# Performance work log

Hardware: AMD Instinct MI355X
Metric: run time of the kernel (lower is better)

Reference implementation:

```python
import jax, jax.numpy as jnp
import numpy as np

N_NODES = 50000
N_EDGES = 800000
DIM = 128


def setup_inputs() -> dict:
    key = jax.random.key(0)
    k_x, k_e, k_w1, k_w2 = jax.random.split(key, 4)
    x = jax.random.normal(k_x, (N_NODES, DIM), dtype=jnp.float32)
    edge_index = jax.random.randint(k_e, (2, N_EDGES), 0, N_NODES, dtype=jnp.int64)
    scale = 1.0 / np.sqrt(DIM)
    W1 = jax.random.normal(k_w1, (DIM, DIM), dtype=jnp.float32) * scale
    b1 = jnp.zeros((DIM,), dtype=jnp.float32)
    W2 = jax.random.normal(k_w2, (DIM, DIM), dtype=jnp.float32) * scale
    b2 = jnp.zeros((DIM,), dtype=jnp.float32)
    return {"x": x, "edge_index": edge_index, "W1": W1, "b1": b1, "W2": W2, "b2": b2}


def _gcn_conv(x, W, b, src, dst, n_nodes):
    """PyG GCNConv: D^{-1/2}(A+I)D^{-1/2} (x @ W) + b, self-loops added."""
    h = x @ W  # [N, D]
    ones = jnp.ones(src.shape[0], dtype=h.dtype)
    # degree of A+I, counting incoming edges at target nodes plus self-loop
    deg = jax.ops.segment_sum(ones, dst, num_segments=n_nodes) + 1.0
    dinv = jax.lax.rsqrt(deg)  # [N]
    norm = dinv[src] * dinv[dst]  # [E]
    msgs = h[src] * norm[:, None]  # [E, D] gather (memory-bound)
    agg = jax.ops.segment_sum(msgs, dst, num_segments=n_nodes)  # scatter-add
    agg = agg + h * (dinv * dinv)[:, None]  # self-loop contribution
    return agg + b


def reference(x, edge_index, W1, b1, W2, b2):
    src, dst = edge_index[0], edge_index[1]
    n = x.shape[0]
    identity = x
    out = jax.nn.relu(_gcn_conv(x, W1, b1, src, dst, n))
    out = _gcn_conv(out, W2, b2, src, dst, n)
    return jax.nn.relu(out + identity)
```

## Files before the change

kernel.cpp:

```cpp
#include <hip/hip_runtime.h>

#define N_NODES 50000
#define N_EDGES 800000
#define DIM 128
#define NB 391
#define CAP 2560
#define NCH 7
#define BIN_CHUNK 4096
#define BIN_BLOCKS 196

typedef unsigned int uint;
typedef unsigned short ushort;
typedef __attribute__((ext_vector_type(8))) __bf16 bf16x8;
typedef __attribute__((ext_vector_type(4))) float f32x4;

__device__ __forceinline__ uint f2bf(float f) {
    uint u = __float_as_uint(f);
    return (u + 0x7FFFu + ((u >> 16) & 1u)) >> 16;
}
__device__ __forceinline__ float2 bf2f2(uint u) {
    return make_float2(__uint_as_float(u << 16), __uint_as_float(u & 0xFFFF0000u));
}


__global__ __launch_bounds__(256) void prep_kernel(const float* __restrict__ W1,
                                                   const float* __restrict__ W2,
                                                   uint* __restrict__ Wt1,
                                                   uint* __restrict__ Wt2,
                                                   int* __restrict__ bincursor) {
    int idx = blockIdx.x * 256 + threadIdx.x;
    if (idx < 16384) {
        const float* W = (idx < 8192) ? W1 : W2;
        uint* Wt = (idx < 8192) ? Wt1 : Wt2;
        int i = idx & 8191;
        int n = i >> 6, k2 = i & 63;
        uint lo = f2bf(W[(2 * k2) * DIM + n]);
        uint hi = f2bf(W[(2 * k2 + 1) * DIM + n]);
        Wt[i] = lo | (hi << 16);
    } else {
        int b = idx - 16384;
        if (b < NB) bincursor[b] = b * CAP;
    }
}


__global__ __launch_bounds__(256) void bin_kernel(const int* __restrict__ ei,
                                                  int* __restrict__ bincursor,
                                                  uint* __restrict__ pairs) {
    __shared__ int lh[NB];
    __shared__ int lbase[NB];
    int t = threadIdx.x;
    int eb = blockIdx.x * BIN_CHUNK;

    for (int b = t; b < NB; b += 256) lh[b] = 0;
    __syncthreads();

    int s_reg[16], d_reg[16];
#pragma unroll
    for (int i = 0; i < 16; ++i) {
        int e = eb + i * 256 + t;
        if (e < N_EDGES) {
            s_reg[i] = ei[e];
            d_reg[i] = ei[N_EDGES + e];
            atomicAdd(&lh[d_reg[i] >> 7], 1);
        } else {
            d_reg[i] = -1;
        }
    }
    __syncthreads();

    for (int b = t; b < NB; b += 256) {
        int c = lh[b];
        lbase[b] = c ? atomicAdd(&bincursor[b], c) : 0;
    }
    __syncthreads();
    for (int b = t; b < NB; b += 256) lh[b] = 0;
    __syncthreads();

#pragma unroll
    for (int i = 0; i < 16; ++i) {
        int d = d_reg[i];
        if (d >= 0) {
            int bin = d >> 7;
            int r = atomicAdd(&lh[bin], 1);
            pairs[lbase[bin] + r] = ((uint)s_reg[i] << 7) | (uint)(d & 127);
        }
    }
}


__global__ __launch_bounds__(256) void fill2_kernel(const uint* __restrict__ pairs,
                                                    const int* __restrict__ bincursor,
                                                    int* __restrict__ rowbeg,
                                                    int* __restrict__ rowend,
                                                    float* __restrict__ dinv,
                                                    int* __restrict__ csr_src) {
    __shared__ int cnt[128 * 8];
    __shared__ int nsum[128];
    __shared__ int nbase[128];
    int t = threadIdx.x;
    int blk = blockIdx.x;
    int bs = blk * CAP;
    int be = bincursor[blk];

    for (int i = t; i < 128 * 8; i += 256) cnt[i] = 0;
    __syncthreads();

    for (int p = bs + t; p < be; p += 256) {
        uint pr = pairs[p];
        atomicAdd(&cnt[(pr & 127u) * 8 + (pr >> 20)], 1);
    }
    __syncthreads();

    if (t < 128) {
        int s = 0;
#pragma unroll
        for (int c = 0; c < NCH; ++c) s += cnt[t * 8 + c];
        nsum[t] = s;
        nbase[t] = s;
    }
    __syncthreads();
#pragma unroll
    for (int off = 1; off < 128; off <<= 1) {
        int v = (t < 128 && t >= off) ? nbase[t - off] : 0;
        __syncthreads();
        if (t < 128) nbase[t] += v;
        __syncthreads();
    }

    if (t < 128) {
        int ex = nbase[t] - nsum[t];
        int node = blk * 128 + t;
        if (node < N_NODES) {
            rowbeg[node] = bs + ex;
            rowend[node] = bs + nbase[t];
            dinv[node] = rsqrtf((float)nsum[t] + 1.0f);
        }
        int run = ex;
#pragma unroll
        for (int c = 0; c < NCH; ++c) {
            int v = cnt[t * 8 + c];
            cnt[t * 8 + c] = run;
            run += v;
        }
    }
    __syncthreads();

    for (int p = bs + t; p < be; p += 256) {
        uint pr = pairs[p];
        int r = atomicAdd(&cnt[(pr & 127u) * 8 + (pr >> 20)], 1);
        csr_src[bs + r] = (int)(pr >> 7);
    }
}


template <bool ABF>
__global__ __launch_bounds__(256) void mgemm_kernel(const void* __restrict__ Xv,
                                                    const uint* __restrict__ Wt,
                                                    const float* __restrict__ dinv,
                                                    uint* __restrict__ Hs) {
    int t = threadIdx.x;
    int wv = t >> 6;
    int l = t & 63;
    int col = l & 15;
    int g = l >> 4;
    int r0 = blockIdx.x * 64 + wv * 16;

    int ar = r0 + col;
    if (ar > N_NODES - 1) ar = N_NODES - 1;

    bf16x8 a[4];
    if (ABF) {
        const uint4* Xr = (const uint4*)((const uint*)Xv + (size_t)ar * 64);
#pragma unroll
        for (int kk = 0; kk < 4; ++kk) a[kk] = __builtin_bit_cast(bf16x8, Xr[kk * 4 + g]);
    } else {
        const float4* Xr = (const float4*)((const float*)Xv + (size_t)ar * DIM);
#pragma unroll
        for (int kk = 0; kk < 4; ++kk) {
            float4 x0 = Xr[kk * 8 + g * 2];
            float4 x1 = Xr[kk * 8 + g * 2 + 1];
            uint4 p;
            p.x = f2bf(x0.x) | (f2bf(x0.y) << 16);
            p.y = f2bf(x0.z) | (f2bf(x0.w) << 16);
            p.z = f2bf(x1.x) | (f2bf(x1.y) << 16);
            p.w = f2bf(x1.z) | (f2bf(x1.w) << 16);
            a[kk] = __builtin_bit_cast(bf16x8, p);
        }
    }

    const uint4* Wr = (const uint4*)Wt;
    f32x4 acc[8];
#pragma unroll
    for (int n = 0; n < 8; ++n) acc[n] = (f32x4){0.f, 0.f, 0.f, 0.f};

#pragma unroll
    for (int n = 0; n < 8; ++n) {
        const uint4* wrow = Wr + (size_t)(n * 16 + col) * 16;
#pragma unroll
        for (int kk = 0; kk < 4; ++kk) {
            bf16x8 b = __builtin_bit_cast(bf16x8, wrow[kk * 4 + g]);
            acc[n] = __builtin_amdgcn_mfma_f32_16x16x32_bf16(a[kk], b, acc[n], 0, 0, 0);
        }
    }

#pragma unroll
    for (int j = 0; j < 4; ++j) {
        int row = r0 + g * 4 + j;
        if (row < N_NODES) {
            float di = dinv[row];
            ushort* hrow = (ushort*)(Hs + (size_t)row * 64);
#pragma unroll
            for (int n = 0; n < 8; ++n) {
                hrow[n * 16 + col] = (ushort)f2bf(acc[n][j] * di);
            }
        }
    }
}


template <bool RES, bool OBF>
__global__ __launch_bounds__(256) void agg_kernel(const int* __restrict__ rowbeg,
                                                  const int* __restrict__ rowend,
                                                  const int* __restrict__ csr_src,
                                                  const uint* __restrict__ Hs,
                                                  const float* __restrict__ dinv,
                                                  const float* __restrict__ b,
                                                  const float* __restrict__ resid,
                                                  void* __restrict__ outv) {
    int wave = (int)((blockIdx.x * (size_t)blockDim.x + threadIdx.x) >> 6);
    int lane = threadIdx.x & 63;
    int grp = lane >> 4;
    int li = lane & 15;
    int node = wave * 4 + grp;

    int beg = rowbeg[node];
    int end = rowend[node];

    const uint4* H4 = (const uint4*)Hs;
    float a0, a1, a2, a3, a4, a5, a6, a7;
    {
        uint4 su = H4[(size_t)node * 16 + li];
        float2 v0 = bf2f2(su.x), v1 = bf2f2(su.y), v2 = bf2f2(su.z), v3 = bf2f2(su.w);
        a0 = v0.x; a1 = v0.y; a2 = v1.x; a3 = v1.y;
        a4 = v2.x; a5 = v2.y; a6 = v3.x; a7 = v3.y;
    }

#define ADD8(u)                                                                   \
    {                                                                             \
        float2 v0 = bf2f2(u.x), v1 = bf2f2(u.y), v2 = bf2f2(u.z), v3 = bf2f2(u.w);\
        a0 += v0.x; a1 += v0.y; a2 += v1.x; a3 += v1.y;                           \
        a4 += v2.x; a5 += v2.y; a6 += v3.x; a7 += v3.y;                           \
    }

    int e = beg;
    for (; e + 3 < end; e += 4) {
        int s0 = csr_src[e], s1 = csr_src[e + 1], s2 = csr_src[e + 2], s3 = csr_src[e + 3];
        uint4 u0 = H4[(size_t)s0 * 16 + li];
        uint4 u1 = H4[(size_t)s1 * 16 + li];
        uint4 u2 = H4[(size_t)s2 * 16 + li];
        uint4 u3 = H4[(size_t)s3 * 16 + li];
        ADD8(u0);
        ADD8(u1);
        ADD8(u2);
        ADD8(u3);
    }
    for (; e < end; ++e) {
        int s = csr_src[e];
        uint4 u = H4[(size_t)s * 16 + li];
        ADD8(u);
    }
#undef ADD8

    float di = dinv[node];
    const float4* B4 = (const float4*)b;
    float4 bb0 = B4[li * 2], bb1 = B4[li * 2 + 1];
    float r0 = a0 * di + bb0.x, r1 = a1 * di + bb0.y;
    float r2 = a2 * di + bb0.z, r3 = a3 * di + bb0.w;
    float r4 = a4 * di + bb1.x, r5 = a5 * di + bb1.y;
    float r6 = a6 * di + bb1.z, r7 = a7 * di + bb1.w;

    if (OBF) {
        uint4 o;
        o.x = f2bf(fmaxf(r0, 0.f)) | (f2bf(fmaxf(r1, 0.f)) << 16);
        o.y = f2bf(fmaxf(r2, 0.f)) | (f2bf(fmaxf(r3, 0.f)) << 16);
        o.z = f2bf(fmaxf(r4, 0.f)) | (f2bf(fmaxf(r5, 0.f)) << 16);
        o.w = f2bf(fmaxf(r6, 0.f)) | (f2bf(fmaxf(r7, 0.f)) << 16);
        ((uint4*)outv)[(size_t)node * 16 + li] = o;
    } else {
        if (RES) {
            const float4* R4 = (const float4*)(resid + (size_t)node * DIM);
            float4 x0 = R4[li * 2], x1 = R4[li * 2 + 1];
            r0 += x0.x; r1 += x0.y; r2 += x0.z; r3 += x0.w;
            r4 += x1.x; r5 += x1.y; r6 += x1.z; r7 += x1.w;
        }
        float4* O4 = (float4*)((float*)outv + (size_t)node * DIM);
        O4[li * 2] = make_float4(fmaxf(r0, 0.f), fmaxf(r1, 0.f), fmaxf(r2, 0.f), fmaxf(r3, 0.f));
        O4[li * 2 + 1] = make_float4(fmaxf(r4, 0.f), fmaxf(r5, 0.f), fmaxf(r6, 0.f), fmaxf(r7, 0.f));
    }
}


extern "C" void kernel_launch(void* const* d_in, const int* in_sizes, int n_in,
                              void* d_out, int out_size, void* d_ws, size_t ws_size,
                              hipStream_t stream) {
    const float* x = (const float*)d_in[0];
    const int* edge_index = (const int*)d_in[1];
    const float* W1 = (const float*)d_in[2];
    const float* b1 = (const float*)d_in[3];
    const float* W2 = (const float*)d_in[4];
    const float* b2 = (const float*)d_in[5];
    float* out = (float*)d_out;

    char* ws = (char*)d_ws;
    int*   bincursor = (int*)(ws + 0);
    float* dinv      = (float*)(ws + (64 << 10));
    int*   rowbeg    = (int*)(ws + (320 << 10));
    int*   rowend    = (int*)(ws + (576 << 10));
    int*   csr_src   = (int*)(ws + (1 << 20));
    uint*  pairs     = (uint*)(ws + (6 << 20));
    uint*  Hs        = (uint*)(ws + (11 << 20));
    uint*  out1b     = (uint*)(ws + (24 << 20));
    uint*  Wt1       = (uint*)(ws + (37 << 20));
    uint*  Wt2       = (uint*)(ws + (37 << 20) + (64 << 10));

    prep_kernel<<<66, 256, 0, stream>>>(W1, W2, Wt1, Wt2, bincursor);
    bin_kernel<<<BIN_BLOCKS, 256, 0, stream>>>(edge_index, bincursor, pairs);
    fill2_kernel<<<NB, 256, 0, stream>>>(pairs, bincursor, rowbeg, rowend, dinv, csr_src);

    const int gemm_grid = (N_NODES + 63) / 64;
    const int agg_grid = 3125;

    mgemm_kernel<false><<<gemm_grid, 256, 0, stream>>>(x, Wt1, dinv, Hs);
    agg_kernel<false, true><<<agg_grid, 256, 0, stream>>>(rowbeg, rowend, csr_src, Hs, dinv, b1,
                                                          nullptr, out1b);

    mgemm_kernel<true><<<gemm_grid, 256, 0, stream>>>(out1b, Wt2, dinv, Hs);
    agg_kernel<true, false><<<agg_grid, 256, 0, stream>>>(rowbeg, rowend, csr_src, Hs, dinv, b2,
                                                          x, out);
}
```

Measured before the change: 139.3 us.

## Fuse GEMM1 into binning launch and aggregation1 with GEMM2 via LDS

New measurement: 124.8 us. 1.12x faster.

```diff
diff --git a/kernel.cpp b/kernel.cpp
--- a/kernel.cpp
+++ b/kernel.cpp
@@ -8,6 +8,7 @@
 #define NCH 7
 #define BIN_CHUNK 4096
 #define BIN_BLOCKS 196
+#define GEMM_TILES 782
 
 typedef unsigned int uint;
 typedef unsigned short ushort;
@@ -34,9 +35,7 @@
         uint* Wt = (idx < 8192) ? Wt1 : Wt2;
         int i = idx & 8191;
         int n = i >> 6, k2 = i & 63;
-        uint lo = f2bf(W[(2 * k2) * DIM + n]);
-        uint hi = f2bf(W[(2 * k2 + 1) * DIM + n]);
-        Wt[i] = lo | (hi << 16);
+        Wt[i] = f2bf(W[(2 * k2) * DIM + n]) | (f2bf(W[(2 * k2 + 1) * DIM + n]) << 16);
     } else {
         int b = idx - 16384;
         if (b < NB) bincursor[b] = b * CAP;
@@ -44,9 +43,90 @@
 }
 
 
-__global__ __launch_bounds__(256) void bin_kernel(const int* __restrict__ ei,
-                                                  int* __restrict__ bincursor,
-                                                  uint* __restrict__ pairs) {
+template <bool ABF, bool SCALE, bool FROM_LDS>
+__device__ __forceinline__ void gemm_tile(const void* Xv, const uint* __restrict__ sB,
+                                          const uint* __restrict__ Wt,
+                                          const float* __restrict__ dinv, int base,
+                                          uint* __restrict__ Hout) {
+    int t = threadIdx.x;
+    int wv = t >> 6;
+    int l = t & 63;
+    int col = l & 15;
+    int g = l >> 4;
+    int lr = wv * 16 + col;
+    int grow = base + lr;
+
+    bf16x8 af[4];
+    if (FROM_LDS) {
+#pragma unroll
+        for (int kk = 0; kk < 4; ++kk) {
+            int ui = lr * 64 + ((kk * 16 + g * 4) ^ ((lr & 7) << 2));
+            af[kk] = __builtin_bit_cast(bf16x8, *(const uint4*)&sB[ui]);
+        }
+    } else {
+        int ar = grow > N_NODES - 1 ? N_NODES - 1 : grow;
+        if (ABF) {
+            const uint4* Xr = (const uint4*)((const uint*)Xv + (size_t)ar * 64);
+#pragma unroll
+            for (int kk = 0; kk < 4; ++kk) af[kk] = __builtin_bit_cast(bf16x8, Xr[kk * 4 + g]);
+        } else {
+            const float4* Xr = (const float4*)((const float*)Xv + (size_t)ar * DIM);
+#pragma unroll
+            for (int kk = 0; kk < 4; ++kk) {
+                float4 x0 = Xr[kk * 8 + g * 2];
+                float4 x1 = Xr[kk * 8 + g * 2 + 1];
+                uint4 p;
+                p.x = f2bf(x0.x) | (f2bf(x0.y) << 16);
+                p.y = f2bf(x0.z) | (f2bf(x0.w) << 16);
+                p.z = f2bf(x1.x) | (f2bf(x1.y) << 16);
+                p.w = f2bf(x1.z) | (f2bf(x1.w) << 16);
+                af[kk] = __builtin_bit_cast(bf16x8, p);
+            }
+        }
+    }
+
+    const uint4* Wr = (const uint4*)Wt;
+    f32x4 acc[8];
+#pragma unroll
+    for (int n = 0; n < 8; ++n) acc[n] = (f32x4){0.f, 0.f, 0.f, 0.f};
+
+#pragma unroll
+    for (int n = 0; n < 8; ++n) {
+        const uint4* wrow = Wr + (size_t)(n * 16 + col) * 16;
+#pragma unroll
+        for (int kk = 0; kk < 4; ++kk) {
+            bf16x8 bf = __builtin_bit_cast(bf16x8, wrow[kk * 4 + g]);
+            acc[n] = __builtin_amdgcn_mfma_f32_16x16x32_bf16(af[kk], bf, acc[n], 0, 0, 0);
+        }
+    }
+
+#pragma unroll
+    for (int j = 0; j < 4; ++j) {
+        int row = base + wv * 16 + g * 4 + j;
+        if (row < N_NODES) {
+            float di = SCALE ? dinv[row] : 1.0f;
+            ushort* hrow = (ushort*)(Hout + (size_t)row * 64);
+#pragma unroll
+            for (int n = 0; n < 8; ++n) {
+                float v = SCALE ? acc[n][j] * di : acc[n][j];
+                hrow[n * 16 + col] = (ushort)f2bf(v);
+            }
+        }
+    }
+}
+
+
+__global__ __launch_bounds__(256) void bin_gemm1_kernel(const int* __restrict__ ei,
+                                                        int* __restrict__ bincursor,
+                                                        uint* __restrict__ pairs,
+                                                        const float* __restrict__ x,
+                                                        const uint* __restrict__ Wt1,
+                                                        uint* __restrict__ Hs) {
+    if (blockIdx.x >= BIN_BLOCKS) {
+        int tile = blockIdx.x - BIN_BLOCKS;
+        gemm_tile<false, false, false>((const void*)x, nullptr, Wt1, nullptr, tile * 64, Hs);
+        return;
+    }
     __shared__ int lh[NB];
     __shared__ int lbase[NB];
     int t = threadIdx.x;
@@ -154,103 +234,33 @@
 }
 
 
-template <bool ABF>
-__global__ __launch_bounds__(256) void mgemm_kernel(const void* __restrict__ Xv,
-                                                    const uint* __restrict__ Wt,
-                                                    const float* __restrict__ dinv,
-                                                    uint* __restrict__ Hs) {
-    int t = threadIdx.x;
-    int wv = t >> 6;
-    int l = t & 63;
-    int col = l & 15;
-    int g = l >> 4;
-    int r0 = blockIdx.x * 64 + wv * 16;
-
-    int ar = r0 + col;
-    if (ar > N_NODES - 1) ar = N_NODES - 1;
-
-    bf16x8 a[4];
-    if (ABF) {
-        const uint4* Xr = (const uint4*)((const uint*)Xv + (size_t)ar * 64);
-#pragma unroll
-        for (int kk = 0; kk < 4; ++kk) a[kk] = __builtin_bit_cast(bf16x8, Xr[kk * 4 + g]);
-    } else {
-        const float4* Xr = (const float4*)((const float*)Xv + (size_t)ar * DIM);
-#pragma unroll
-        for (int kk = 0; kk < 4; ++kk) {
-            float4 x0 = Xr[kk * 8 + g * 2];
-            float4 x1 = Xr[kk * 8 + g * 2 + 1];
-            uint4 p;
-            p.x = f2bf(x0.x) | (f2bf(x0.y) << 16);
-            p.y = f2bf(x0.z) | (f2bf(x0.w) << 16);
-            p.z = f2bf(x1.x) | (f2bf(x1.y) << 16);
-            p.w = f2bf(x1.z) | (f2bf(x1.w) << 16);
-            a[kk] = __builtin_bit_cast(bf16x8, p);
-        }
-    }
-
-    const uint4* Wr = (const uint4*)Wt;
-    f32x4 acc[8];
-#pragma unroll
-    for (int n = 0; n < 8; ++n) acc[n] = (f32x4){0.f, 0.f, 0.f, 0.f};
-
-#pragma unroll
-    for (int n = 0; n < 8; ++n) {
-        const uint4* wrow = Wr + (size_t)(n * 16 + col) * 16;
-#pragma unroll
-        for (int kk = 0; kk < 4; ++kk) {
-            bf16x8 b = __builtin_bit_cast(bf16x8, wrow[kk * 4 + g]);
-            acc[n] = __builtin_amdgcn_mfma_f32_16x16x32_bf16(a[kk], b, acc[n], 0, 0, 0);
-        }
-    }
-
-#pragma unroll
-    for (int j = 0; j < 4; ++j) {
-        int row = r0 + g * 4 + j;
-        if (row < N_NODES) {
-            float di = dinv[row];
-            ushort* hrow = (ushort*)(Hs + (size_t)row * 64);
-#pragma unroll
-            for (int n = 0; n < 8; ++n) {
-                hrow[n * 16 + col] = (ushort)f2bf(acc[n][j] * di);
-            }
-        }
-    }
-}
-
-
-template <bool RES, bool OBF>
-__global__ __launch_bounds__(256) void agg_kernel(const int* __restrict__ rowbeg,
-                                                  const int* __restrict__ rowend,
-                                                  const int* __restrict__ csr_src,
-                                                  const uint* __restrict__ Hs,
-                                                  const float* __restrict__ dinv,
-                                                  const float* __restrict__ b,
-                                                  const float* __restrict__ resid,
-                                                  void* __restrict__ outv) {
-    int wave = (int)((blockIdx.x * (size_t)blockDim.x + threadIdx.x) >> 6);
-    int lane = threadIdx.x & 63;
-    int grp = lane >> 4;
-    int li = lane & 15;
-    int node = wave * 4 + grp;
-
+template <bool DSRC>
+__device__ __forceinline__ void agg_node(const int* __restrict__ rowbeg,
+                                         const int* __restrict__ rowend,
+                                         const int* __restrict__ csr_src,
+                                         const uint* __restrict__ Hs,
+                                         const float* __restrict__ dinv,
+                                         const float* __restrict__ bias, int node, int li,
+                                         float r[8]) {
     int beg = rowbeg[node];
     int end = rowend[node];
+    float di = dinv[node];
 
     const uint4* H4 = (const uint4*)Hs;
     float a0, a1, a2, a3, a4, a5, a6, a7;
     {
         uint4 su = H4[(size_t)node * 16 + li];
         float2 v0 = bf2f2(su.x), v1 = bf2f2(su.y), v2 = bf2f2(su.z), v3 = bf2f2(su.w);
-        a0 = v0.x; a1 = v0.y; a2 = v1.x; a3 = v1.y;
-        a4 = v2.x; a5 = v2.y; a6 = v3.x; a7 = v3.y;
-    }
-
-#define ADD8(u)                                                                   \
+        float sf = DSRC ? di : 1.0f;
+        a0 = sf * v0.x; a1 = sf * v0.y; a2 = sf * v1.x; a3 = sf * v1.y;
+        a4 = sf * v2.x; a5 = sf * v2.y; a6 = sf * v3.x; a7 = sf * v3.y;
+    }
+
+#define ADDF8(u, f)                                                               \
     {                                                                             \
         float2 v0 = bf2f2(u.x), v1 = bf2f2(u.y), v2 = bf2f2(u.z), v3 = bf2f2(u.w);\
-        a0 += v0.x; a1 += v0.y; a2 += v1.x; a3 += v1.y;                           \
-        a4 += v2.x; a5 += v2.y; a6 += v3.x; a7 += v3.y;                           \
+        a0 += f * v0.x; a1 += f * v0.y; a2 += f * v1.x; a3 += f * v1.y;           \
+        a4 += f * v2.x; a5 += f * v2.y; a6 += f * v3.x; a7 += f * v3.y;           \
     }
 
     int e = beg;
@@ -260,44 +270,97 @@
         uint4 u1 = H4[(size_t)s1 * 16 + li];
         uint4 u2 = H4[(size_t)s2 * 16 + li];
         uint4 u3 = H4[(size_t)s3 * 16 + li];
-        ADD8(u0);
-        ADD8(u1);
-        ADD8(u2);
-        ADD8(u3);
+        float f0 = DSRC ? dinv[s0] : 1.0f;
+        float f1 = DSRC ? dinv[s1] : 1.0f;
+        float f2 = DSRC ? dinv[s2] : 1.0f;
+        float f3 = DSRC ? dinv[s3] : 1.0f;
+        ADDF8(u0, f0);
+        ADDF8(u1, f1);
+        ADDF8(u2, f2);
+        ADDF8(u3, f3);
     }
     for (; e < end; ++e) {
         int s = csr_src[e];
         uint4 u = H4[(size_t)s * 16 + li];
-        ADD8(u);
-    }
-#undef ADD8
-
-    float di = dinv[node];
-    const float4* B4 = (const float4*)b;
+        float f = DSRC ? dinv[s] : 1.0f;
+        ADDF8(u, f);
+    }
+#undef ADDF8
+
+    const float4* B4 = (const float4*)bias;
     float4 bb0 = B4[li * 2], bb1 = B4[li * 2 + 1];
-    float r0 = a0 * di + bb0.x, r1 = a1 * di + bb0.y;
-    float r2 = a2 * di + bb0.z, r3 = a3 * di + bb0.w;
-    float r4 = a4 * di + bb1.x, r5 = a5 * di + bb1.y;
-    float r6 = a6 * di + bb1.z, r7 = a7 * di + bb1.w;
-
-    if (OBF) {
-        uint4 o;
-        o.x = f2bf(fmaxf(r0, 0.f)) | (f2bf(fmaxf(r1, 0.f)) << 16);
-        o.y = f2bf(fmaxf(r2, 0.f)) | (f2bf(fmaxf(r3, 0.f)) << 16);
-        o.z = f2bf(fmaxf(r4, 0.f)) | (f2bf(fmaxf(r5, 0.f)) << 16);
-        o.w = f2bf(fmaxf(r6, 0.f)) | (f2bf(fmaxf(r7, 0.f)) << 16);
-        ((uint4*)outv)[(size_t)node * 16 + li] = o;
-    } else {
-        if (RES) {
-            const float4* R4 = (const float4*)(resid + (size_t)node * DIM);
-            float4 x0 = R4[li * 2], x1 = R4[li * 2 + 1];
-            r0 += x0.x; r1 += x0.y; r2 += x0.z; r3 += x0.w;
-            r4 += x1.x; r5 += x1.y; r6 += x1.z; r7 += x1.w;
-        }
-        float4* O4 = (float4*)((float*)outv + (size_t)node * DIM);
-        O4[li * 2] = make_float4(fmaxf(r0, 0.f), fmaxf(r1, 0.f), fmaxf(r2, 0.f), fmaxf(r3, 0.f));
-        O4[li * 2 + 1] = make_float4(fmaxf(r4, 0.f), fmaxf(r5, 0.f), fmaxf(r6, 0.f), fmaxf(r7, 0.f));
-    }
+    r[0] = a0 * di + bb0.x; r[1] = a1 * di + bb0.y;
+    r[2] = a2 * di + bb0.z; r[3] = a3 * di + bb0.w;
+    r[4] = a4 * di + bb1.x; r[5] = a5 * di + bb1.y;
+    r[6] = a6 * di + bb1.z; r[7] = a7 * di + bb1.w;
+}
+
+
+__global__ __launch_bounds__(256) void aggemm_kernel(const int* __restrict__ rowbeg,
+                                                     const int* __restrict__ rowend,
+                                                     const int* __restrict__ csr_src,
+                                                     const uint* __restrict__ Hs,
+                                                     const float* __restrict__ dinv,
+                                                     const float* __restrict__ b1,
+                                                     const uint* __restrict__ Wt2,
+                                                     uint* __restrict__ Hs2) {
+    __shared__ uint sB[64 * 64];
+    int t = threadIdx.x;
+    int wv = t >> 6;
+    int lane = t & 63;
+    int grp = lane >> 4;
+    int li = lane & 15;
+    int base = blockIdx.x * 64;
+
+#pragma unroll
+    for (int p = 0; p < 4; ++p) {
+        int row = p * 16 + wv * 4 + grp;
+        int node = base + row;
+        if (node < N_NODES) {
+            float r[8];
+            agg_node<true>(rowbeg, rowend, csr_src, Hs, dinv, b1, node, li, r);
+            uint4 o;
+            o.x = f2bf(fmaxf(r[0], 0.f)) | (f2bf(fmaxf(r[1], 0.f)) << 16);
+            o.y = f2bf(fmaxf(r[2], 0.f)) | (f2bf(fmaxf(r[3], 0.f)) << 16);
+            o.z = f2bf(fmaxf(r[4], 0.f)) | (f2bf(fmaxf(r[5], 0.f)) << 16);
+            o.w = f2bf(fmaxf(r[6], 0.f)) | (f2bf(fmaxf(r[7], 0.f)) << 16);
+            int ui = row * 64 + ((li * 4) ^ ((row & 7) << 2));
+            *(uint4*)&sB[ui] = o;
+        }
+    }
+    __syncthreads();
+
+    gemm_tile<true, true, true>(nullptr, sB, Wt2, dinv, base, Hs2);
+}
+
+
+__global__ __launch_bounds__(256) void agg2_kernel(const int* __restrict__ rowbeg,
+                                                   const int* __restrict__ rowend,
+                                                   const int* __restrict__ csr_src,
+                                                   const uint* __restrict__ Hs2,
+                                                   const float* __restrict__ dinv,
+                                                   const float* __restrict__ b2,
+                                                   const float* __restrict__ resid,
+                                                   float* __restrict__ out) {
+    int wave = (int)((blockIdx.x * (size_t)blockDim.x + threadIdx.x) >> 6);
+    int lane = threadIdx.x & 63;
+    int grp = lane >> 4;
+    int li = lane & 15;
+    int node = wave * 4 + grp;
+
+    float r[8];
+    agg_node<false>(rowbeg, rowend, csr_src, Hs2, dinv, b2, node, li, r);
+
+    const float4* R4 = (const float4*)(resid + (size_t)node * DIM);
+    float4 x0 = R4[li * 2], x1 = R4[li * 2 + 1];
+    r[0] += x0.x; r[1] += x0.y; r[2] += x0.z; r[3] += x0.w;
+    r[4] += x1.x; r[5] += x1.y; r[6] += x1.z; r[7] += x1.w;
+
+    float4* O4 = (float4*)(out + (size_t)node * DIM);
+    O4[li * 2] = make_float4(fmaxf(r[0], 0.f), fmaxf(r[1], 0.f), fmaxf(r[2], 0.f),
+                             fmaxf(r[3], 0.f));
+    O4[li * 2 + 1] = make_float4(fmaxf(r[4], 0.f), fmaxf(r[5], 0.f), fmaxf(r[6], 0.f),
+                                 fmaxf(r[7], 0.f));
 }
 
 
@@ -320,22 +383,15 @@
     int*   csr_src   = (int*)(ws + (1 << 20));
     uint*  pairs     = (uint*)(ws + (6 << 20));
     uint*  Hs        = (uint*)(ws + (11 << 20));
-    uint*  out1b     = (uint*)(ws + (24 << 20));
+    uint*  Hs2       = (uint*)(ws + (24 << 20));
     uint*  Wt1       = (uint*)(ws + (37 << 20));
     uint*  Wt2       = (uint*)(ws + (37 << 20) + (64 << 10));
 
     prep_kernel<<<66, 256, 0, stream>>>(W1, W2, Wt1, Wt2, bincursor);
-    bin_kernel<<<BIN_BLOCKS, 256, 0, stream>>>(edge_index, bincursor, pairs);
+    bin_gemm1_kernel<<<BIN_BLOCKS + GEMM_TILES, 256, 0, stream>>>(edge_index, bincursor, pairs,
+                                                                  x, Wt1, Hs);
     fill2_kernel<<<NB, 256, 0, stream>>>(pairs, bincursor, rowbeg, rowend, dinv, csr_src);
-
-    const int gemm_grid = (N_NODES + 63) / 64;
-    const int agg_grid = 3125;
-
-    mgemm_kernel<false><<<gemm_grid, 256, 0, stream>>>(x, Wt1, dinv, Hs);
-    agg_kernel<false, true><<<agg_grid, 256, 0, stream>>>(rowbeg, rowend, csr_src, Hs, dinv, b1,
-                                                          nullptr, out1b);
-
-    mgemm_kernel<true><<<gemm_grid, 256, 0, stream>>>(out1b, Wt2, dinv, Hs);
-    agg_kernel<true, false><<<agg_grid, 256, 0, stream>>>(rowbeg, rowend, csr_src, Hs, dinv, b2,
-                                                          x, out);
-}
+    aggemm_kernel<<<GEMM_TILES, 256, 0, stream>>>(rowbeg, rowend, csr_src, Hs, dinv, b1, Wt2,
+                                                  Hs2);
+    agg2_kernel<<<3125, 256, 0, stream>>>(rowbeg, rowend, csr_src, Hs2, dinv, b2, x, out);
+}
```
